# Kernel optimization log

Measured on AMD Instinct MI355X. Metric: run time of the kernel, lower is better.

The kernel has to match this reference:

```python
import jax, jax.numpy as jnp
import numpy as np

N = 256    # num_nodes = 2*K*R
K = 16     # num_cluster (after reflection pairing)
R = 8      # ratio = size of each original cluster
IN = 32
OUT = 32
BS = 32


def setup_inputs() -> dict:
    key = jax.random.key(0)
    k1, k2, k3, k4 = jax.random.split(key, 4)
    x = jax.random.normal(k1, (BS, N, IN), dtype=jnp.float32)
    w_diag = jax.random.uniform(k2, (IN * OUT, K), dtype=jnp.float32)           # torch.rand
    w_off = jax.random.uniform(k3, (IN * OUT, K, 2 * K), dtype=jnp.float32)     # torch.rand
    stdv = 1.0 / np.sqrt(OUT)
    b1 = jax.random.uniform(k4, (OUT,), minval=-stdv, maxval=stdv, dtype=jnp.float32)
    perm = np.random.default_rng(0).permutation(N)   # flatten_ids of shuffled clusters
    permute_ids = jnp.asarray(perm, dtype=jnp.int32)
    inv_permute = jnp.asarray(np.argsort(perm), dtype=jnp.int32)
    return {"x": x, "w_diag": w_diag, "w_off": w_off, "b1": b1,
            "permute_ids": permute_ids, "inv_permute": inv_permute}


def _build_W(w_diag, w_off):
    # Faithful to: kron(tie_weights(w_off), ones(R,R))/N + kron(diag_embed(repeat_interleave(w_diag,2)), eye(R))
    C = w_diag.shape[0]            # in*out channels
    width = 2 * K
    # tie_weights: interleave original rows with pair-swapped-column rows
    swap = np.arange(width).reshape(-1, 2)[:, ::-1].reshape(-1)      # [1,0,3,2,...]
    tied = jnp.stack([w_off, w_off[:, :, swap]], axis=2).reshape(C, width, width)
    # kron with ones(R,R) == repeat each entry R times along both node axes
    W3 = jnp.repeat(jnp.repeat(tied, R, axis=1), R, axis=2) / N      # (C, N, N)
    # kron(diag_embed(.), eye(R)) == add per-node diagonal, constant within cluster
    wd_full = jnp.repeat(jnp.repeat(w_diag, 2, axis=1), R, axis=1)   # (C, N)
    di = jnp.arange(N)
    W3 = W3.at[:, di, di].add(wd_full)
    # rearrange '(o i) j k -> (o j) (i k)'
    return W3.reshape(OUT, IN, N, N).transpose(0, 2, 1, 3).reshape(OUT * N, IN * N)


def reference(x, w_diag, w_off, b1, permute_ids, inv_permute):
    W = _build_W(w_diag, w_off)                       # (OUT*N, IN*N)
    xp = x[:, permute_ids, :]                         # (BS, N, IN) permuted
    xp = xp.transpose(0, 2, 1).reshape(BS, IN * N)    # feature-major flatten
    out = xp @ W.T                                    # (BS, OUT*N)
    out = out.reshape(BS, OUT, N).transpose(0, 2, 1)  # (BS, N, OUT)
    out = out[:, inv_permute, :] + b1[None, None, :]
    return out
```

## Files before the change

### kernel.cpp

```cpp
#include <hip/hip_runtime.h>

#define N_   256
#define IN_  32
#define OUT_ 32
#define BS_  32

__global__ __launch_bounds__(256) void k_fused(const float* __restrict__ x,
                                               const int* __restrict__ perm,
                                               const float* __restrict__ w_off,
                                               const float* __restrict__ w_diag,
                                               const float* __restrict__ b1,
                                               float* __restrict__ out) {
    const int t = threadIdx.x;
    const int b = blockIdx.x;
    const int s  = b >> 3;
    const int og = b & 7;

    __shared__ int   perm_s[256];
    __shared__ float xp[256 * 36];
    __shared__ float yT[32 * 36];
    __shared__ float wdt[16 * 128];
    __shared__ float part[128 * 5];
    __shared__ float z_l[128];

    perm_s[t] = perm[t];
    __syncthreads();

    {
        const int r0 = t >> 3;
        const int c  = (t & 7) * 4;
#pragma unroll
        for (int pass = 0; pass < 8; ++pass) {
            const int r = pass * 32 + r0;
            const float4 v = *(const float4*)(x + (s * N_ + perm_s[r]) * IN_ + c);
            *(float4*)&xp[r * 36 + c] = v;
        }
    }
    {
        const int o_l = t >> 6;
        const int i   = (t >> 1) & 31;
        const int o   = og * 4 + o_l;
#pragma unroll
        for (int k = 0; k < 2; ++k) {
            const int uq = (t & 1) * 2 + k;
            const float4 v = *(const float4*)(w_diag + (o * 32 + i) * 16 + uq * 4);
            wdt[(uq * 4 + 0) * 128 + o_l * 32 + i] = v.x;
            wdt[(uq * 4 + 1) * 128 + o_l * 32 + i] = v.y;
            wdt[(uq * 4 + 2) * 128 + o_l * 32 + i] = v.z;
            wdt[(uq * 4 + 3) * 128 + o_l * 32 + i] = v.w;
        }
    }
    __syncthreads();

    {
        const int i  = t & 31;
        const int qb = t >> 5;
#pragma unroll
        for (int k = 0; k < 4; ++k) {
            const int q = qb * 4 + k;
            float sum = 0.f;
#pragma unroll
            for (int j = 0; j < 8; ++j)
                sum += xp[(8 * q + j) * 36 + i];
            yT[i * 36 + q] = sum;
        }
    }
    __syncthreads();

    {
        const int u   = t & 15;
        const int o_l = (t >> 4) & 3;
        const int qq  = t >> 6;
        const int o   = og * 4 + o_l;
        const float* wbase = w_off + ((o * 32) * 16 + u) * 32 + qq * 8;
        const float* yb    = yT + qq * 8;
        float p0 = 0.f, p1 = 0.f;
#pragma unroll
        for (int i = 0; i < 32; ++i) {
            const float4 w0 = *(const float4*)(wbase + i * 512);
            const float4 w1 = *(const float4*)(wbase + i * 512 + 4);
            const float4 ya = *(const float4*)(yb + i * 36);
            const float4 yc = *(const float4*)(yb + i * 36 + 4);
            p0 += w0.x*ya.x + w0.y*ya.y + w0.z*ya.z + w0.w*ya.w
                + w1.x*yc.x + w1.y*yc.y + w1.z*yc.z + w1.w*yc.w;
            p1 += w0.y*ya.x + w0.x*ya.y + w0.w*ya.z + w0.z*ya.w
                + w1.y*yc.x + w1.x*yc.y + w1.w*yc.z + w1.z*yc.w;
        }
        const int slot = (o_l * 16 + u) * 2;
        part[(slot + 0) * 5 + qq] = p0;
        part[(slot + 1) * 5 + qq] = p1;
    }
    __syncthreads();

    if (t < 128) {
        const float sum = part[t * 5 + 0] + part[t * 5 + 1]
                        + part[t * 5 + 2] + part[t * 5 + 3];
        const int o_l = t >> 5;
        z_l[t] = sum * (1.0f / 256.0f) + b1[og * 4 + o_l];
    }
    __syncthreads();

    {
        const int r = t;
        const int u = r >> 4;
        const int p = (r >> 3) & 1;
        const float4* xr = (const float4*)&xp[r * 36];
        float4 xv[8];
#pragma unroll
        for (int ii = 0; ii < 8; ++ii) xv[ii] = xr[ii];

        float acc[4];
#pragma unroll
        for (int o_l = 0; o_l < 4; ++o_l) {
            float a = z_l[(o_l * 16 + u) * 2 + p];
            const float4* wr = (const float4*)&wdt[u * 128 + o_l * 32];
#pragma unroll
            for (int ii = 0; ii < 8; ++ii) {
                const float4 w = wr[ii];
                a += xv[ii].x*w.x + xv[ii].y*w.y + xv[ii].z*w.z + xv[ii].w*w.w;
            }
            acc[o_l] = a;
        }
        const float4 res = make_float4(acc[0], acc[1], acc[2], acc[3]);
        *(float4*)(out + (s * N_ + perm_s[r]) * OUT_ + og * 4) = res;
    }
}

extern "C" void kernel_launch(void* const* d_in, const int* in_sizes, int n_in,
                              void* d_out, int out_size, void* d_ws, size_t ws_size,
                              hipStream_t stream) {
    const float* x      = (const float*)d_in[0];
    const float* w_diag = (const float*)d_in[1];
    const float* w_off  = (const float*)d_in[2];
    const float* b1     = (const float*)d_in[3];
    const int*   perm   = (const int*)d_in[4];

    float* out = (float*)d_out;
    k_fused<<<256, 256, 0, stream>>>(x, perm, w_off, w_diag, b1, out);
}
```

Baseline: 74.83 us.

## Quadruple block size to 1024 threads and split each stage's work finer

Raises the block from 256 to 1024 threads and redistributes every stage so each thread does a quarter of the work. The gather, the cluster sums and the diagonal term each get one element per thread, and the off-diagonal reduction is split over 16 partial sums across the input-channel halves and q-groups. The goal is more latency hiding per block, since the grid is only 256 blocks. The cost is more partial-sum traffic and reduction work, scalar rather than float4 output stores, and higher register and scheduling pressure from 1024-thread blocks.

New measurement: 69.55 us. 7.1% less time.

```diff
diff --git a/kernel.cpp b/kernel.cpp
--- a/kernel.cpp
+++ b/kernel.cpp
@@ -5,12 +5,12 @@
 #define OUT_ 32
 #define BS_  32
 
-__global__ __launch_bounds__(256) void k_fused(const float* __restrict__ x,
-                                               const int* __restrict__ perm,
-                                               const float* __restrict__ w_off,
-                                               const float* __restrict__ w_diag,
-                                               const float* __restrict__ b1,
-                                               float* __restrict__ out) {
+__global__ __launch_bounds__(1024) void k_fused(const float* __restrict__ x,
+                                                const int* __restrict__ perm,
+                                                const float* __restrict__ w_off,
+                                                const float* __restrict__ w_diag,
+                                                const float* __restrict__ b1,
+                                                float* __restrict__ out) {
     const int t = threadIdx.x;
     const int b = blockIdx.x;
     const int s  = b >> 3;
@@ -19,110 +19,94 @@
     __shared__ int   perm_s[256];
     __shared__ float xp[256 * 36];
     __shared__ float yT[32 * 36];
-    __shared__ float wdt[16 * 128];
-    __shared__ float part[128 * 5];
+    __shared__ float wdt[64 * 36];
+    __shared__ float part[128 * 17];
     __shared__ float z_l[128];
 
-    perm_s[t] = perm[t];
+    if (t < 256) perm_s[t] = perm[t];
     __syncthreads();
 
     {
+        const int c4 = t & 7;
         const int r0 = t >> 3;
-        const int c  = (t & 7) * 4;
 #pragma unroll
-        for (int pass = 0; pass < 8; ++pass) {
-            const int r = pass * 32 + r0;
-            const float4 v = *(const float4*)(x + (s * N_ + perm_s[r]) * IN_ + c);
-            *(float4*)&xp[r * 36 + c] = v;
+        for (int pass = 0; pass < 2; ++pass) {
+            const int r = pass * 128 + r0;
+            const float4 v = *(const float4*)(x + (s * N_ + perm_s[r]) * IN_ + c4 * 4);
+            *(float4*)&xp[r * 36 + c4 * 4] = v;
         }
     }
-    {
-        const int o_l = t >> 6;
-        const int i   = (t >> 1) & 31;
+    if (t < 512) {
+        const int uq  = t & 3;
+        const int row = t >> 2;
+        const int o_l = row >> 5;
+        const int i   = row & 31;
         const int o   = og * 4 + o_l;
-#pragma unroll
-        for (int k = 0; k < 2; ++k) {
-            const int uq = (t & 1) * 2 + k;
-            const float4 v = *(const float4*)(w_diag + (o * 32 + i) * 16 + uq * 4);
-            wdt[(uq * 4 + 0) * 128 + o_l * 32 + i] = v.x;
-            wdt[(uq * 4 + 1) * 128 + o_l * 32 + i] = v.y;
-            wdt[(uq * 4 + 2) * 128 + o_l * 32 + i] = v.z;
-            wdt[(uq * 4 + 3) * 128 + o_l * 32 + i] = v.w;
-        }
+        const float4 v = *(const float4*)(w_diag + (o * 32 + i) * 16 + uq * 4);
+        wdt[((uq * 4 + 0) * 4 + o_l) * 36 + i] = v.x;
+        wdt[((uq * 4 + 1) * 4 + o_l) * 36 + i] = v.y;
+        wdt[((uq * 4 + 2) * 4 + o_l) * 36 + i] = v.z;
+        wdt[((uq * 4 + 3) * 4 + o_l) * 36 + i] = v.w;
     }
     __syncthreads();
 
     {
-        const int i  = t & 31;
-        const int qb = t >> 5;
+        const int i = t & 31;
+        const int q = t >> 5;
+        float sum = 0.f;
 #pragma unroll
-        for (int k = 0; k < 4; ++k) {
-            const int q = qb * 4 + k;
-            float sum = 0.f;
-#pragma unroll
-            for (int j = 0; j < 8; ++j)
-                sum += xp[(8 * q + j) * 36 + i];
-            yT[i * 36 + q] = sum;
-        }
+        for (int j = 0; j < 8; ++j)
+            sum += xp[(8 * q + j) * 36 + i];
+        yT[i * 36 + q] = sum;
     }
     __syncthreads();
 
     {
-        const int u   = t & 15;
-        const int o_l = (t >> 4) & 3;
-        const int qq  = t >> 6;
+        const int qq  = t & 7;
+        const int u   = (t >> 3) & 15;
+        const int o_l = (t >> 7) & 3;
+        const int ih  = t >> 9;
         const int o   = og * 4 + o_l;
-        const float* wbase = w_off + ((o * 32) * 16 + u) * 32 + qq * 8;
-        const float* yb    = yT + qq * 8;
+        const float* wbase = w_off + ((o * 32 + ih * 16) * 16 + u) * 32 + qq * 4;
+        const float* yb    = yT + (ih * 16) * 36 + qq * 4;
         float p0 = 0.f, p1 = 0.f;
 #pragma unroll
-        for (int i = 0; i < 32; ++i) {
-            const float4 w0 = *(const float4*)(wbase + i * 512);
-            const float4 w1 = *(const float4*)(wbase + i * 512 + 4);
-            const float4 ya = *(const float4*)(yb + i * 36);
-            const float4 yc = *(const float4*)(yb + i * 36 + 4);
-            p0 += w0.x*ya.x + w0.y*ya.y + w0.z*ya.z + w0.w*ya.w
-                + w1.x*yc.x + w1.y*yc.y + w1.z*yc.z + w1.w*yc.w;
-            p1 += w0.y*ya.x + w0.x*ya.y + w0.w*ya.z + w0.z*ya.w
-                + w1.y*yc.x + w1.x*yc.y + w1.w*yc.z + w1.z*yc.w;
+        for (int ii = 0; ii < 16; ++ii) {
+            const float4 w  = *(const float4*)(wbase + ii * 512);
+            const float4 ya = *(const float4*)(yb + ii * 36);
+            p0 += w.x * ya.x + w.y * ya.y + w.z * ya.z + w.w * ya.w;
+            p1 += w.y * ya.x + w.x * ya.y + w.w * ya.z + w.z * ya.w;
         }
         const int slot = (o_l * 16 + u) * 2;
-        part[(slot + 0) * 5 + qq] = p0;
-        part[(slot + 1) * 5 + qq] = p1;
+        const int k    = ih * 8 + qq;
+        part[(slot + 0) * 17 + k] = p0;
+        part[(slot + 1) * 17 + k] = p1;
     }
     __syncthreads();
 
     if (t < 128) {
-        const float sum = part[t * 5 + 0] + part[t * 5 + 1]
-                        + part[t * 5 + 2] + part[t * 5 + 3];
-        const int o_l = t >> 5;
-        z_l[t] = sum * (1.0f / 256.0f) + b1[og * 4 + o_l];
+        float sum = 0.f;
+#pragma unroll
+        for (int k = 0; k < 16; ++k) sum += part[t * 17 + k];
+        z_l[t] = sum * (1.0f / 256.0f) + b1[og * 4 + (t >> 5)];
     }
     __syncthreads();
 
     {
-        const int r = t;
-        const int u = r >> 4;
-        const int p = (r >> 3) & 1;
+        const int o_l = t & 3;
+        const int r   = t >> 2;
+        const int u   = r >> 4;
+        const int p   = (r >> 3) & 1;
+        float acc = z_l[(o_l * 16 + u) * 2 + p];
         const float4* xr = (const float4*)&xp[r * 36];
-        float4 xv[8];
+        const float4* wr = (const float4*)&wdt[(u * 4 + o_l) * 36];
 #pragma unroll
-        for (int ii = 0; ii < 8; ++ii) xv[ii] = xr[ii];
-
-        float acc[4];
-#pragma unroll
-        for (int o_l = 0; o_l < 4; ++o_l) {
-            float a = z_l[(o_l * 16 + u) * 2 + p];
-            const float4* wr = (const float4*)&wdt[u * 128 + o_l * 32];
-#pragma unroll
-            for (int ii = 0; ii < 8; ++ii) {
-                const float4 w = wr[ii];
-                a += xv[ii].x*w.x + xv[ii].y*w.y + xv[ii].z*w.z + xv[ii].w*w.w;
-            }
-            acc[o_l] = a;
+        for (int ii = 0; ii < 8; ++ii) {
+            const float4 xv = xr[ii];
+            const float4 wv = wr[ii];
+            acc += xv.x * wv.x + xv.y * wv.y + xv.z * wv.z + xv.w * wv.w;
         }
-        const float4 res = make_float4(acc[0], acc[1], acc[2], acc[3]);
-        *(float4*)(out + (s * N_ + perm_s[r]) * OUT_ + og * 4) = res;
+        out[(s * N_ + perm_s[r]) * OUT_ + og * 4 + o_l] = acc;
     }
 }
 
@@ -136,5 +120,5 @@
     const int*   perm   = (const int*)d_in[4];
 
     float* out = (float*)d_out;
-    k_fused<<<256, 256, 0, stream>>>(x, perm, w_off, w_diag, b1, out);
+    k_fused<<<256, 1024, 0, stream>>>(x, perm, w_off, w_diag, b1, out);
 }
```
